# Performance work log

Hardware: AMD Instinct MI355X
Metric: run time of the kernel (lower is better)

## Reference

```python
import jax, jax.numpy as jnp
import numpy as np
import math

B, N, D, H = 4, 2048, 1024, 16
d = D // H
F = 2048                      # field_size
PAD = 8192                    # _next_fast_size(4*F) = 2^13
FB = PAD // 2 + 1             # rfft freq bins
NC = 32                       # spectral-gate control points
EPS = 1e-6                    # feature-map positivity floor


def setup_inputs():
    key = jax.random.key(0)
    ks = jax.random.split(key, 16)
    rn = lambda k, sh, s=0.02: (jax.random.normal(k, sh) * s).astype(jnp.float32)
    eye = jnp.eye(d, dtype=jnp.float32)
    n = jnp.arange(H, dtype=jnp.float32)
    return {
        "x": jax.random.normal(ks[0], (B, N, D), dtype=jnp.float32),
        "w_qkvg": rn(ks[1], (4 * D, D)),
        "b_qkvg": jnp.concatenate([jnp.zeros(3 * D), jnp.full((D,), 2.0)]).astype(jnp.float32),
        "w_out": rn(ks[2], (D, D)),
        "b_out": jnp.zeros((D,), jnp.float32),
        "qfm_w": jnp.stack([eye + rn(ks[3], (d, d)), eye + rn(ks[4], (d, d))]),
        "qfm_b": jnp.zeros((2, d), jnp.float32),
        "kfm_w": jnp.stack([eye + rn(ks[5], (d, d)), eye + rn(ks[6], (d, d))]),
        "kfm_b": jnp.zeros((2, d), jnp.float32),
        "wg_w": rn(ks[7], (1, d)),
        "wg_b": jnp.zeros((1,), jnp.float32),
        "ln_g": jnp.ones((d,), jnp.float32),
        "ln_b": jnp.zeros((d,), jnp.float32),
        "sg_w1": rn(ks[8], (D, D)),
        "sg_b1": jnp.zeros((D,), jnp.float32),
        "sg_w2": rn(ks[9], (H * NC, D), 0.001),
        "sg_b2": jnp.zeros((H * NC,), jnp.float32),
        "wave_freq": (math.pi * (2 * n + 1) / 2).astype(jnp.float32),
        "wave_damp": jnp.full((H,), -0.69, jnp.float32),
        "wave_phase": jnp.linspace(0.0, math.pi, H).astype(jnp.float32),
        "coupling": (jnp.eye(H, dtype=jnp.float32) + rn(ks[10], (H, H), 0.01)),
    }


def _featmap(x, w, b):
    # Hedgehog-style learned positive feature map: depth x (Linear -> ReLU), + eps
    for i in range(w.shape[0]):
        x = jax.nn.relu(x @ w[i].T + b[i])
    return x + EPS


def reference(x, w_qkvg, b_qkvg, w_out, b_out, qfm_w, qfm_b, kfm_w, kfm_b,
              wg_w, wg_b, ln_g, ln_b, sg_w1, sg_b1, sg_w2, sg_b2,
              wave_freq, wave_damp, wave_phase, coupling):
    # fused qkvg projection -> per-head tensors (B,H,N,d)
    qkvg = x @ w_qkvg.T + b_qkvg
    q, k, v, g = [t.reshape(B, N, H, d).transpose(0, 2, 1, 3)
                  for t in jnp.split(qkvg, 4, axis=-1)]
    phi_q = _featmap(q, qfm_w, qfm_b)
    phi_k = _featmap(k, kfm_w, kfm_b)
    wg = jax.nn.sigmoid(k @ wg_w.T + wg_b)  # (B,H,N,1) write gate

    # token -> field position mapping (cached buffers in the original)
    stride = (F - 1) / max(N - 1, 1)
    pos = jnp.clip(jnp.arange(N, dtype=jnp.float32) * stride, 0, F - 2)
    lo = jnp.clip(pos.astype(jnp.int32), 0, F - 2)
    hi = lo + 1
    frac = jnp.clip(pos - lo.astype(jnp.float32), 0.0, 1.0)

    # scatter numerator (gated phi_k*v) + denominator (gated phi_k) streams
    write = jnp.concatenate([wg * phi_k * v, wg * phi_k], axis=-1)  # (B,H,N,2d)
    field = jnp.zeros((B, H, F, 2 * d), jnp.float32)
    field = field.at[:, :, lo, :].add(write * (1.0 - frac)[:, None])
    field = field.at[:, :, hi, :].add(write * frac[:, None])

    # left-aligned causal damped-wave kernel per head
    t = jnp.arange(F, dtype=jnp.float32) / F
    kern = jnp.exp(-jnp.exp(wave_damp)[:, None] * t) * \
           jnp.cos(wave_freq[:, None] * t + wave_phase[:, None])  # (H,F)
    base_fft = jnp.fft.rfft(kern, n=PAD, axis=-1)                 # (H,FB) complex

    # content-adaptive spectral gate from token 0 (causally safe)
    q0 = q[:, :, 0, :]
    mu = q0.mean(-1, keepdims=True)
    var = q0.var(-1, keepdims=True)
    q0 = (q0 - mu) / jnp.sqrt(var + 1e-5) * ln_g + ln_b
    h1 = jax.nn.gelu(q0.reshape(B, H * d) @ sg_w1.T + sg_b1)
    ctrl = (h1 @ sg_w2.T + sg_b2).reshape(B, H, NC)
    ip = jnp.arange(FB, dtype=jnp.float32) * (NC - 1) / (FB - 1)  # align_corners=True
    il = jnp.clip(ip.astype(jnp.int32), 0, NC - 2)
    iw = ip - il.astype(jnp.float32)
    gate = ctrl[:, :, il] * (1.0 - iw) + ctrl[:, :, il + 1] * iw  # (B,H,FB)
    mod = base_fft[None] * (1.0 + gate)                           # (B,H,FB) complex

    # FFT-domain global convolution + head coupling
    conv = jnp.fft.irfft(jnp.fft.rfft(field, n=PAD, axis=2) * mod[..., None],
                         n=PAD, axis=2)[:, :, :F, :]
    conv = jnp.einsum('hg,bgfc->bhfc', coupling, conv)

    # linear-interp read-back at token positions
    y = conv[:, :, lo, :] * (1.0 - frac)[:, None] + conv[:, :, hi, :] * frac[:, None]
    y_num, y_den = y[..., :d], y[..., d:]
    den = jnp.abs(jnp.sum(phi_q * y_den, axis=-1, keepdims=True)) + 1e-4
    out_h = (phi_q * y_num / den) * jax.nn.sigmoid(g)
    return out_h.transpose(0, 2, 1, 3).reshape(B, N, D) @ w_out.T + b_out
```

## Files before the change

### kernel.cpp

```cpp
#include <hip/hip_runtime.h>
#include <math.h>

#define B_   4
#define N_   2048
#define D_   1024
#define H_   16
#define d_   64
#define F_   2048
#define PAD_ 8192
#define FB_  4097
#define NC_  32
#define EPS_ 1e-6f
#define PI_F 3.14159265358979323846f
#define PI_D 3.14159265358979323846

typedef unsigned short ushort_t;
typedef short bf16x8 __attribute__((ext_vector_type(8)));
typedef float f32x4  __attribute__((ext_vector_type(4)));

#define GLD16(gp, lp) __builtin_amdgcn_global_load_lds( \
    (const __attribute__((address_space(1))) unsigned int*)(const void*)(gp), \
    (__attribute__((address_space(3))) unsigned int*)(void*)(lp), 16, 0, 0)

__device__ __forceinline__ ushort_t bf16_rne(float v) {
    unsigned b = __float_as_uint(v);
    unsigned rb = b + 0x7fffu + ((b >> 16) & 1u);
    return (ushort_t)(rb >> 16);
}
__device__ __forceinline__ void split_bf16(float v, ushort_t& h, ushort_t& l) {
    h = bf16_rne(v);
    float fh = __uint_as_float((unsigned)h << 16);
    l = bf16_rne(v - fh);
}

__device__ __forceinline__ float2 cmul(float2 a, float2 w) {
    return make_float2(a.x * w.x - a.y * w.y, a.x * w.y + a.y * w.x);
}
__device__ __forceinline__ float2 cmulc(float2 a, float2 w) {
    return make_float2(a.x * w.x + a.y * w.y, a.y * w.x - a.x * w.y);
}

__global__ __launch_bounds__(256) void kern_twid(float2* __restrict__ twid,
                                                 float2* __restrict__ tw4) {
    int idx = blockIdx.x * 256 + threadIdx.x;
    if (idx < 13 * 4096) {
        const int lh = idx >> 12, t = idx & 4095;
        const int hh = 1 << lh;
        const int j = t & (hh - 1);
        double s, c;
        sincos(-PI_D * (double)j / (double)hh, &s, &c);
        twid[idx] = make_float2((float)c, (float)s);
    } else {
        idx -= 13 * 4096;
        if (idx < 6 * 3072) {
            const int s = idx / 3072;
            const int r = idx - s * 3072;
            const int j = r / 3;
            const int m = r - 3 * j + 1;
            const int q = 1024 >> (2 * s);
            double sn, cs;
            sincos(-2.0 * PI_D * (double)(m * (j & (q - 1))) / (double)(4 * q), &sn, &cs);
            tw4[idx] = make_float2((float)cs, (float)sn);
        }
    }
}

__global__ __launch_bounds__(256) void kern_split3(
        const float* __restrict__ s0, ushort_t* __restrict__ h0, ushort_t* __restrict__ l0, int n0,
        const float* __restrict__ s1, ushort_t* __restrict__ h1, ushort_t* __restrict__ l1, int n1,
        const float* __restrict__ s2, ushort_t* __restrict__ h2, ushort_t* __restrict__ l2, int n2) {
    int i = blockIdx.x * 256 + threadIdx.x;
    const float* s; ushort_t* hh; ushort_t* ll; int k;
    if (i < n0)                { s = s0; hh = h0; ll = l0; k = i; }
    else if (i < n0 + n1)      { s = s1; hh = h1; ll = l1; k = i - n0; }
    else if (i < n0 + n1 + n2) { s = s2; hh = h2; ll = l2; k = i - n0 - n1; }
    else return;
    ushort_t h, l;
    split_bf16(s[k], h, l);
    hh[k] = h; ll[k] = l;
}

__global__ __launch_bounds__(256) void gemm_mfma(
        const ushort_t* __restrict__ Ah, const ushort_t* __restrict__ Al, int lda,
        const ushort_t* __restrict__ Bh, const ushort_t* __restrict__ Bl, int ldb,
        const float* __restrict__ bias, float* __restrict__ C,
        int Nn, int K) {
    __shared__ __align__(16) ushort_t At0[128 * 32];
    __shared__ __align__(16) ushort_t At1[128 * 32];
    __shared__ __align__(16) ushort_t Bt0[128 * 32];
    __shared__ __align__(16) ushort_t Bt1[128 * 32];

    const int tid = threadIdx.x;
    const int wv = tid >> 6, lane = tid & 63;
    const int quad = lane >> 4, lrow = lane & 15;
    const int m0 = blockIdx.y * 128, n0 = blockIdx.x * 128;
    const int mw = (wv >> 1) * 64, nw = (wv & 1) * 64;

    const int srow = lane >> 2;
    const int schunk = (((lane & 3) ^ ((lane >> 3) & 3)) * 8);
    const int qsw = ((quad ^ ((lrow >> 1) & 3)) * 8);

    f32x4 acc[4][4] = {};

    for (int k0 = 0; k0 < K; k0 += 32) {
        {
            const size_t ga = (size_t)(m0 + wv * 32 + srow) * lda + k0 + schunk;
            const size_t gb = (size_t)(n0 + wv * 32 + srow) * ldb + k0 + schunk;
            const size_t ga2 = ga + (size_t)16 * lda;
            const size_t gb2 = gb + (size_t)16 * ldb;
            GLD16(Ah + ga,  &At0[(wv * 32) * 32]);
            GLD16(Ah + ga2, &At0[(wv * 32 + 16) * 32]);
            GLD16(Al + ga,  &At1[(wv * 32) * 32]);
            GLD16(Al + ga2, &At1[(wv * 32 + 16) * 32]);
            GLD16(Bh + gb,  &Bt0[(wv * 32) * 32]);
            GLD16(Bh + gb2, &Bt0[(wv * 32 + 16) * 32]);
            GLD16(Bl + gb,  &Bt1[(wv * 32) * 32]);
            GLD16(Bl + gb2, &Bt1[(wv * 32 + 16) * 32]);
        }
        __syncthreads();

        bf16x8 a0[4], a1[4], b0[4], b1[4];
#pragma unroll
        for (int i = 0; i < 4; ++i) {
            a0[i] = *(const bf16x8*)&At0[(mw + i * 16 + lrow) * 32 + qsw];
            a1[i] = *(const bf16x8*)&At1[(mw + i * 16 + lrow) * 32 + qsw];
            b0[i] = *(const bf16x8*)&Bt0[(nw + i * 16 + lrow) * 32 + qsw];
            b1[i] = *(const bf16x8*)&Bt1[(nw + i * 16 + lrow) * 32 + qsw];
        }
#pragma unroll
        for (int mi = 0; mi < 4; ++mi)
#pragma unroll
            for (int nj = 0; nj < 4; ++nj) {
                acc[mi][nj] = __builtin_amdgcn_mfma_f32_16x16x32_bf16(a0[mi], b0[nj], acc[mi][nj], 0, 0, 0);
                acc[mi][nj] = __builtin_amdgcn_mfma_f32_16x16x32_bf16(a0[mi], b1[nj], acc[mi][nj], 0, 0, 0);
                acc[mi][nj] = __builtin_amdgcn_mfma_f32_16x16x32_bf16(a1[mi], b0[nj], acc[mi][nj], 0, 0, 0);
            }
        __syncthreads();
    }

#pragma unroll
    for (int mi = 0; mi < 4; ++mi) {
        const int row = m0 + mw + mi * 16 + quad * 4;
#pragma unroll
        for (int nj = 0; nj < 4; ++nj) {
            const int col = n0 + nw + nj * 16 + lrow;
            const float bv = bias[col];
#pragma unroll
            for (int r = 0; r < 4; ++r)
                C[(size_t)(row + r) * Nn + col] = acc[mi][nj][r] + bv;
        }
    }
}

__device__ __forceinline__ float gelu_f(float x) {
    return 0.5f * x * (1.f + tanhf(0.7978845608028654f * (x + 0.044715f * x * x * x)));
}

__global__ __launch_bounds__(256) void kern_gemv4(const float* __restrict__ A,
                                                  const float* __restrict__ W,
                                                  const float* __restrict__ bias,
                                                  float* __restrict__ C,
                                                  int Nn, int act) {
    const int tid = threadIdx.x;
    const int wv = tid >> 6, lane = tid & 63;
    const int col = blockIdx.x * 4 + wv;
    const float* wp = W + (size_t)col * D_;
    float a0 = 0.f, a1 = 0.f, a2 = 0.f, a3 = 0.f;
#pragma unroll
    for (int i = 0; i < 16; ++i) {
        int k = lane + i * 64;
        float w = wp[k];
        a0 += A[k] * w;
        a1 += A[D_ + k] * w;
        a2 += A[2 * D_ + k] * w;
        a3 += A[3 * D_ + k] * w;
    }
    for (int m = 1; m < 64; m <<= 1) {
        a0 += __shfl_xor(a0, m);
        a1 += __shfl_xor(a1, m);
        a2 += __shfl_xor(a2, m);
        a3 += __shfl_xor(a3, m);
    }
    if (lane == 0) {
        float bv = bias[col];
        float v0 = a0 + bv, v1 = a1 + bv, v2 = a2 + bv, v3 = a3 + bv;
        if (act) { v0 = gelu_f(v0); v1 = gelu_f(v1); v2 = gelu_f(v2); v3 = gelu_f(v3); }
        C[0 * Nn + col] = v0;
        C[1 * Nn + col] = v1;
        C[2 * Nn + col] = v2;
        C[3 * Nn + col] = v3;
    }
}

__global__ __launch_bounds__(256) void kern_feat(float* __restrict__ qkvg,
                                                 const float* __restrict__ qfm_w,
                                                 const float* __restrict__ qfm_b,
                                                 const float* __restrict__ kfm_w,
                                                 const float* __restrict__ kfm_b,
                                                 const float* __restrict__ wg_w,
                                                 const float* __restrict__ wg_b,
                                                 float* __restrict__ field) {
    __shared__ __align__(16) float in_t[64][68];
    __shared__ __align__(16) float tmp[64][68];
    __shared__ __align__(16) float wbuf[64][68];
    __shared__ __align__(16) float bsm[64];
    __shared__ float wsm[64];
    __shared__ float wgbuf[64];

    const int tid = threadIdx.x;
    const int lane = tid & 63, grp = tid >> 6;
    const int n0 = blockIdx.x * 64;
    const int h = blockIdx.y, b = blockIdx.z;
    const size_t rowbase = (size_t)(b * N_ + n0) * 4096;

    const int lr4 = tid >> 4;
    const int lc4 = (tid & 15) * 4;

    const int rg = lane >> 4;
    const int cg4 = (lane & 15) * 4;
    const int rbase = grp * 16 + rg * 4;

#define LOAD64x64(dst, off) \
    for (int it = 0; it < 4; ++it) { \
        int r = lr4 + it * 16; \
        float4 v = *(const float4*)&qkvg[rowbase + (size_t)r * 4096 + (off) + lc4]; \
        *(float4*)&dst[r][lc4] = v; \
    }

#define MLP2_ACC(srcarr) \
    f32x4 acc[4] = {}; \
    for (int c4 = 0; c4 < 64; c4 += 4) { \
        f32x4 wv0 = *(const f32x4*)&wbuf[c4 + 0][cg4]; \
        f32x4 wv1 = *(const f32x4*)&wbuf[c4 + 1][cg4]; \
        f32x4 wv2 = *(const f32x4*)&wbuf[c4 + 2][cg4]; \
        f32x4 wv3 = *(const f32x4*)&wbuf[c4 + 3][cg4]; \
        _Pragma("unroll") for (int rr = 0; rr < 4; ++rr) { \
            f32x4 iv = *(const f32x4*)&srcarr[rbase + rr][c4]; \
            acc[rr] += wv0 * iv[0]; \
            acc[rr] += wv1 * iv[1]; \
            acc[rr] += wv2 * iv[2]; \
            acc[rr] += wv3 * iv[3]; \
        } \
    }

#define MLP2_STORE_LDS(dstarr, EPSV) { \
    f32x4 b4 = *(const f32x4*)&bsm[cg4]; \
    _Pragma("unroll") for (int rr = 0; rr < 4; ++rr) { \
        f32x4 v = acc[rr] + b4; \
        _Pragma("unroll") for (int k = 0; k < 4; ++k) v[k] = fmaxf(v[k], 0.f) + (EPSV); \
        *(f32x4*)&dstarr[rbase + rr][cg4] = v; } }

    LOAD64x64(in_t, D_ + h * 64)
    for (int it = 0; it < 16; ++it) {
        int r = grp + 4 * it;
        wbuf[lane][r] = kfm_w[(size_t)r * 64 + lane];
    }
    if (tid < 64) { bsm[tid] = kfm_b[tid]; wsm[tid] = wg_w[tid]; }
    __syncthreads();
    if (tid < 64) {
        float s = 0.f;
        for (int c4 = 0; c4 < 64; c4 += 4) {
            float4 iv = *(const float4*)&in_t[tid][c4];
            s += iv.x * wsm[c4] + iv.y * wsm[c4 + 1] + iv.z * wsm[c4 + 2] + iv.w * wsm[c4 + 3];
        }
        s += wg_b[0];
        wgbuf[tid] = 1.f / (1.f + expf(-s));
    }
    {
        MLP2_ACC(in_t)
        MLP2_STORE_LDS(tmp, 0.f)
    }
    __syncthreads();
    for (int it = 0; it < 16; ++it) {
        int r = grp + 4 * it;
        wbuf[lane][r] = kfm_w[(size_t)(64 + r) * 64 + lane];
    }
    if (tid < 64) bsm[tid] = kfm_b[64 + tid];
    __syncthreads();
    {
        MLP2_ACC(tmp)
        MLP2_STORE_LDS(in_t, EPS_)
    }
    __syncthreads();
    LOAD64x64(tmp, 2 * D_ + h * 64)
    __syncthreads();

    {
        float* frow = field + (size_t)(b * H_ + h) * 128 * F_;
        const bool last = (n0 == N_ - 64);
        for (int c = grp; c < 128; c += 4) {
            int i = lane;
            float v = (c < 64) ? wgbuf[i] * in_t[i][c] * tmp[i][c]
                               : wgbuf[i] * in_t[i][c - 64];
            if (last) {
                if (i == 62) {
                    float v2 = (c < 64) ? wgbuf[63] * in_t[63][c] * tmp[63][c]
                                        : wgbuf[63] * in_t[63][c - 64];
                    v += v2;
                } else if (i == 63) v = 0.f;
            }
            frow[(size_t)c * F_ + n0 + i] = v;
        }
    }
    __syncthreads();

    LOAD64x64(in_t, h * 64)
    for (int it = 0; it < 16; ++it) {
        int r = grp + 4 * it;
        wbuf[lane][r] = qfm_w[(size_t)r * 64 + lane];
    }
    if (tid < 64) bsm[tid] = qfm_b[tid];
    __syncthreads();
    {
        MLP2_ACC(in_t)
        MLP2_STORE_LDS(tmp, 0.f)
    }
    __syncthreads();
    for (int it = 0; it < 16; ++it) {
        int r = grp + 4 * it;
        wbuf[lane][r] = qfm_w[(size_t)(64 + r) * 64 + lane];
    }
    if (tid < 64) bsm[tid] = qfm_b[64 + tid];
    __syncthreads();
    {
        MLP2_ACC(tmp)
        f32x4 b4 = *(const f32x4*)&bsm[cg4];
#pragma unroll
        for (int rr = 0; rr < 4; ++rr) {
            f32x4 v = acc[rr] + b4;
#pragma unroll
            for (int k = 0; k < 4; ++k) v[k] = fmaxf(v[k], 0.f) + EPS_;
            *(f32x4*)&qkvg[rowbase + (size_t)(rbase + rr) * 4096 + D_ + h * 64 + cg4] = v;
        }
    }
#undef LOAD64x64
#undef MLP2_ACC
#undef MLP2_STORE_LDS
}

__global__ void kern_ln(const float* __restrict__ qkvg,
                        const float* __restrict__ ln_g,
                        const float* __restrict__ ln_b,
                        float* __restrict__ q0n) {
    const int bh = blockIdx.x, c = threadIdx.x;
    const int b = bh >> 4, h = bh & 15;
    float x = qkvg[(size_t)(b * N_) * 4096 + h * 64 + c];
    float mu = x;
    for (int m = 1; m < 64; m <<= 1) mu += __shfl_xor(mu, m);
    mu *= (1.f / 64.f);
    float dv = (x - mu) * (x - mu);
    for (int m = 1; m < 64; m <<= 1) dv += __shfl_xor(dv, m);
    float var = dv * (1.f / 64.f);
    q0n[b * 1024 + h * 64 + c] = (x - mu) * rsqrtf(var + 1e-5f) * ln_g[c] + ln_b[c];
}

template <int NT>
__device__ __forceinline__ void fft_fwd_dif_t(float* xr, float* xi, int tid, int logn,
                                              const float2* __restrict__ twid) {
    const int nb = 1 << (logn - 1);
    for (int lh = logn - 1; lh >= 0; --lh) {
        const int hh = 1 << lh;
        const float2* tws = twid + lh * 4096;
        for (int t = tid; t < nb; t += NT) {
            int j = t & (hh - 1);
            int i1 = ((t >> lh) << (lh + 1)) | j;
            int i2 = i1 + hh;
            float2 tw = tws[t];
            float ar = xr[i1], ai = xi[i1];
            float br = xr[i2], bi = xi[i2];
            xr[i1] = ar + br; xi[i1] = ai + bi;
            float tr = ar - br, ti = ai - bi;
            xr[i2] = tr * tw.x - ti * tw.y;
            xi[i2] = tr * tw.y + ti * tw.x;
        }
        __syncthreads();
    }
}

template <int NT>
__device__ __forceinline__ void fft_inv_dit_t(float* xr, float* xi, int tid, int logn,
                                              const float2* __restrict__ twid) {
    const int nb = 1 << (logn - 1);
    for (int lh = 0; lh < logn; ++lh) {
        const int hh = 1 << lh;
        const float2* tws = twid + lh * 4096;
        for (int t = tid; t < nb; t += NT) {
            int j = t & (hh - 1);
            int i1 = ((t >> lh) << (lh + 1)) | j;
            int i2 = i1 + hh;
            float2 tw = tws[t];
            float br = xr[i2], bi = xi[i2];
            float tr = br * tw.x + bi * tw.y;
            float ti = bi * tw.x - br * tw.y;
            float ar = xr[i1], ai = xi[i1];
            xr[i1] = ar + tr; xi[i1] = ai + ti;
            xr[i2] = ar - tr; xi[i2] = ai - ti;
        }
        __syncthreads();
    }
}

#define ZIDX(i) ((i) + ((i) >> 4))

template <int NT, int SBEG, int SEND>
__device__ __forceinline__ void fft4_fwd_stages(float2* z, int tid,
                                                const float2* __restrict__ tw4) {
#pragma unroll
    for (int s = SBEG; s < SEND; ++s) {
        const int q = 1024 >> (2 * s);
        const int qq = q + (q >> 4);
        const float2* tws = tw4 + s * 3072;
        for (int t = tid; t < 1024; t += NT) {
            int j = t & (q - 1);
            int base = ((t & ~(q - 1)) << 2) | j;
            int i0, i1, i2, i3;
            if (q >= 16) { i0 = ZIDX(base); i1 = i0 + qq; i2 = i1 + qq; i3 = i2 + qq; }
            else { i0 = ZIDX(base); i1 = ZIDX(base + q); i2 = ZIDX(base + 2 * q); i3 = ZIDX(base + 3 * q); }
            float2 a = z[i0], b = z[i1], c = z[i2], d = z[i3];
            float2 s0 = make_float2(a.x + c.x, a.y + c.y);
            float2 s1 = make_float2(a.x - c.x, a.y - c.y);
            float2 s2 = make_float2(b.x + d.x, b.y + d.y);
            float2 s3 = make_float2(b.x - d.x, b.y - d.y);
            float2 m1 = make_float2(s1.x + s3.y, s1.y - s3.x);
            float2 m2 = make_float2(s0.x - s2.x, s0.y - s2.y);
            float2 m3 = make_float2(s1.x - s3.y, s1.y + s3.x);
            z[i0] = make_float2(s0.x + s2.x, s0.y + s2.y);
            z[i1] = cmul(m1, tws[3 * j + 0]);
            z[i2] = cmul(m2, tws[3 * j + 1]);
            z[i3] = cmul(m3, tws[3 * j + 2]);
        }
        __syncthreads();
    }
}

template <int NT>
__device__ __forceinline__ void fft4_inv(float2* z, int tid,
                                         const float2* __restrict__ tw4) {
#pragma unroll
    for (int s = 5; s >= 0; --s) {
        const int q = 1024 >> (2 * s);
        const int qq = q + (q >> 4);
        const float2* tws = tw4 + s * 3072;
        for (int t = tid; t < 1024; t += NT) {
            int j = t & (q - 1);
            int base = ((t & ~(q - 1)) << 2) | j;
            int i0, i1, i2, i3;
            if (q >= 16) { i0 = ZIDX(base); i1 = i0 + qq; i2 = i1 + qq; i3 = i2 + qq; }
            else { i0 = ZIDX(base); i1 = ZIDX(base + q); i2 = ZIDX(base + 2 * q); i3 = ZIDX(base + 3 * q); }
            float2 a = z[i0];
            float2 b = cmulc(z[i1], tws[3 * j + 0]);
            float2 c = cmulc(z[i2], tws[3 * j + 1]);
            float2 d = cmulc(z[i3], tws[3 * j + 2]);
            float2 p0 = make_float2(a.x + c.x, a.y + c.y);
            float2 p1 = make_float2(a.x - c.x, a.y - c.y);
            float2 p2 = make_float2(b.x + d.x, b.y + d.y);
            float2 p3 = make_float2(b.x - d.x, b.y - d.y);
            z[i0] = make_float2(p0.x + p2.x, p0.y + p2.y);
            z[i1] = make_float2(p1.x - p3.y, p1.y + p3.x);
            z[i2] = make_float2(p0.x - p2.x, p0.y - p2.y);
            z[i3] = make_float2(p1.x + p3.y, p1.y - p3.x);
        }
        __syncthreads();
    }
}

__global__ __launch_bounds__(1024) void kern_prep(const float* __restrict__ freq,
                                                  const float* __restrict__ damp,
                                                  const float* __restrict__ phase,
                                                  const float* __restrict__ ctrl,
                                                  const float2* __restrict__ twid,
                                                  const float2* __restrict__ tw4,
                                                  float* __restrict__ GBR) {
    __shared__ float sm[2 * PAD_];
    float* xr = sm;
    float* xi = sm + PAD_;
    const int bh = blockIdx.x, tid = threadIdx.x;
    const int b = bh >> 4, h = bh & 15;

    const float fr = freq[h], ed = expf(damp[h]), ph = phase[h];
    for (int f = tid; f < PAD_; f += 1024) {
        float v = 0.f;
        if (f < F_) {
            float t = (float)f / (float)F_;
            v = expf(-ed * t) * cosf(fr * t + ph);
        }
        xr[f] = v; xi[f] = 0.f;
    }
    __syncthreads();
    fft_fwd_dif_t<1024>(xr, xi, tid, 13, twid);

    const float* cp = ctrl + b * (H_ * NC_) + h * NC_;
    for (int j = tid; j < PAD_; j += 1024) {
        int k = (int)(__brev((unsigned)j) >> 19);
        int kk = min(k, PAD_ - k);
        float ip = (float)kk * ((float)(NC_ - 1) / (float)(FB_ - 1));
        int il = min((int)ip, NC_ - 2);
        float iw = ip - (float)il;
        float m = 1.f + cp[il] * (1.f - iw) + cp[il + 1] * iw;
        xr[j] *= m;
        xi[j] *= m;
    }
    __syncthreads();
    fft_inv_dit_t<1024>(xr, xi, tid, 13, twid);

    float g[4];
    const float sc = 1.f / (float)PAD_;
#pragma unroll
    for (int u = 0; u < 4; ++u) {
        int j = tid + u * 1024;
        g[u] = ((j < 2048) ? xr[j] : xr[j + 4096]) * sc;
    }
    __syncthreads();
    float2* z = (float2*)sm;
#pragma unroll
    for (int u = 0; u < 4; ++u) {
        int j = tid + u * 1024;
        z[ZIDX(j)] = make_float2(g[u], 0.f);
    }
    __syncthreads();
    fft4_fwd_stages<1024, 0, 5>(z, tid, tw4);
    {
        const float sc2 = 1.f / 4096.f;
        const int t = tid;
        const int base = t << 2;
        float2 a = z[ZIDX(base)], bq = z[ZIDX(base + 1)];
        float2 c = z[ZIDX(base + 2)], dq = z[ZIDX(base + 3)];
        float2 s0 = make_float2(a.x + c.x, a.y + c.y);
        float2 s1 = make_float2(a.x - c.x, a.y - c.y);
        float2 s2 = make_float2(bq.x + dq.x, bq.y + dq.y);
        float2 s3 = make_float2(bq.x - dq.x, bq.y - dq.y);
        float2 o0 = make_float2(s0.x + s2.x, s0.y + s2.y);
        float2 o1 = make_float2(s1.x + s3.y, s1.y - s3.x);
        float2 o2 = make_float2(s0.x - s2.x, s0.y - s2.y);
        float2 o3 = make_float2(s1.x - s3.y, s1.y + s3.x);
        float2* Gp = (float2*)GBR + (size_t)bh * 4096 + base;
        Gp[0] = make_float2(o0.x * sc2, o0.y * sc2);
        Gp[1] = make_float2(o1.x * sc2, o1.y * sc2);
        Gp[2] = make_float2(o2.x * sc2, o2.y * sc2);
        Gp[3] = make_float2(o3.x * sc2, o3.y * sc2);
    }
}

__global__ __launch_bounds__(512) void kern_conv4(float* __restrict__ field,
                                                  const float* __restrict__ GBR,
                                                  const float2* __restrict__ tw4) {
    __shared__ float2 z[4351];
    const int tid = threadIdx.x;
    const int bh = blockIdx.x >> 6, cp = blockIdx.x & 63;
    float* rowx = field + ((size_t)bh * 128 + 2 * cp) * F_;
    float* rowy = rowx + F_;

    for (int f = tid; f < 2048; f += 512)
        z[ZIDX(f)] = make_float2(rowx[f], rowy[f]);
    __syncthreads();

    {
        const float2* tws = tw4;
        for (int t = tid; t < 1024; t += 512) {
            int i0 = ZIDX(t), i1 = i0 + 1088, i2 = i1 + 1088, i3 = i2 + 1088;
            float2 a = z[i0], b = z[i1];
            float2 m1 = make_float2(a.x + b.y, a.y - b.x);
            float2 m2 = make_float2(a.x - b.x, a.y - b.y);
            float2 m3 = make_float2(a.x - b.y, a.y + b.x);
            z[i0] = make_float2(a.x + b.x, a.y + b.y);
            z[i1] = cmul(m1, tws[3 * t + 0]);
            z[i2] = cmul(m2, tws[3 * t + 1]);
            z[i3] = cmul(m3, tws[3 * t + 2]);
        }
        __syncthreads();
    }

    fft4_fwd_stages<512, 1, 5>(z, tid, tw4);

    {
        const float2* G = (const float2*)(GBR) + (size_t)bh * 4096;
        for (int t = tid; t < 1024; t += 512) {
            int base = t << 2;
            int i0 = ZIDX(base), i1 = ZIDX(base + 1), i2 = ZIDX(base + 2), i3 = ZIDX(base + 3);
            float2 a = z[i0], b = z[i1], c = z[i2], d = z[i3];
            float2 s0 = make_float2(a.x + c.x, a.y + c.y);
            float2 s1 = make_float2(a.x - c.x, a.y - c.y);
            float2 s2 = make_float2(b.x + d.x, b.y + d.y);
            float2 s3 = make_float2(b.x - d.x, b.y - d.y);
            float2 o0 = make_float2(s0.x + s2.x, s0.y + s2.y);
            float2 o1 = make_float2(s1.x + s3.y, s1.y - s3.x);
            float2 o2 = make_float2(s0.x - s2.x, s0.y - s2.y);
            float2 o3 = make_float2(s1.x - s3.y, s1.y + s3.x);
            z[i0] = cmul(o0, G[base + 0]);
            z[i1] = cmul(o1, G[base + 1]);
            z[i2] = cmul(o2, G[base + 2]);
            z[i3] = cmul(o3, G[base + 3]);
        }
        __syncthreads();
    }

    fft4_inv<512>(z, tid, tw4);

    for (int f = tid; f < 2048; f += 512) {
        float2 v = z[ZIDX(f)];
        rowx[f] = v.x;
        rowy[f] = v.y;
    }
}

__global__ __launch_bounds__(1024) void kern_combine(float* __restrict__ qkvg,
                                                     const float* __restrict__ field,
                                                     const float* __restrict__ coupling) {
    __shared__ float cpl[16][16];
    __shared__ float sbuf[2][128][17];
    const int tid = threadIdx.x;
    if (tid < 256) cpl[tid >> 4][tid & 15] = coupling[tid];
    const int lane = tid & 63, wv = tid >> 6;
    const int n = blockIdx.x * 16 + wv;
    const int b = blockIdx.y;
    const int f0 = blockIdx.x * 16;
    const int fi = min(n, F_ - 2) - f0;
    const size_t row = (size_t)(b * N_ + n) * 4096;

    const int lc = tid >> 3, lk = (tid & 7) * 2;
    const float* fb = field + (size_t)b * 16 * 128 * F_;

    float2 rv = *(const float2*)&fb[(size_t)lc * F_ + f0 + lk];
    __syncthreads();
    sbuf[0][lc][lk] = rv.x; sbuf[0][lc][lk + 1] = rv.y;

    float ynum[16], yden[16];
#pragma unroll
    for (int hh = 0; hh < 16; ++hh) { ynum[hh] = 0.f; yden[hh] = 0.f; }

    for (int g = 0; g < 16; ++g) {
        if (g < 15)
            rv = *(const float2*)&fb[((size_t)(g + 1) * 128 + lc) * F_ + f0 + lk];
        __syncthreads();
        const float nv = sbuf[g & 1][lane][fi];
        const float dv = sbuf[g & 1][64 + lane][fi];
#pragma unroll
        for (int hh = 0; hh < 16; ++hh) {
            const float cg = cpl[hh][g];
            ynum[hh] += cg * nv;
            yden[hh] += cg * dv;
        }
        if (g < 15) { sbuf[(g + 1) & 1][lc][lk] = rv.x; sbuf[(g + 1) & 1][lc][lk + 1] = rv.y; }
    }

    ushort_t* rp = (ushort_t*)(qkvg + row);
#pragma unroll
    for (int hh = 0; hh < 16; ++hh) {
        float pq = qkvg[row + D_ + hh * 64 + lane];
        float gv = qkvg[row + 3 * D_ + hh * 64 + lane];
        float s = pq * yden[hh];
        for (int m = 1; m < 64; m <<= 1) s += __shfl_xor(s, m);
        float den = fabsf(s) + 1e-4f;
        float o = pq * ynum[hh] / den * (1.f / (1.f + expf(-gv)));
        ushort_t oh, ol;
        split_bf16(o, oh, ol);
        rp[hh * 64 + lane] = oh;
        rp[1024 + hh * 64 + lane] = ol;
    }
}

extern "C" void kernel_launch(void* const* d_in, const int* in_sizes, int n_in,
                              void* d_out, int out_size, void* d_ws, size_t ws_size,
                              hipStream_t stream) {
    const float* x      = (const float*)d_in[0];
    const float* w_qkvg = (const float*)d_in[1];
    const float* b_qkvg = (const float*)d_in[2];
    const float* w_out  = (const float*)d_in[3];
    const float* b_out  = (const float*)d_in[4];
    const float* qfm_w  = (const float*)d_in[5];
    const float* qfm_b  = (const float*)d_in[6];
    const float* kfm_w  = (const float*)d_in[7];
    const float* kfm_b  = (const float*)d_in[8];
    const float* wg_w   = (const float*)d_in[9];
    const float* wg_b   = (const float*)d_in[10];
    const float* ln_g   = (const float*)d_in[11];
    const float* ln_b   = (const float*)d_in[12];
    const float* sg_w1  = (const float*)d_in[13];
    const float* sg_b1  = (const float*)d_in[14];
    const float* sg_w2  = (const float*)d_in[15];
    const float* sg_b2  = (const float*)d_in[16];
    const float* wfreq  = (const float*)d_in[17];
    const float* wdamp  = (const float*)d_in[18];
    const float* wphase = (const float*)d_in[19];
    const float* coup   = (const float*)d_in[20];

    float* ws = (float*)d_ws;
    float*  qkvg   = ws;
    float*  field  = ws + 33554432;
    float*  GBR    = ws + 50593792;
    float2* twid   = (float2*)(ws + 51118080);
    float*  q0n    = ws + 51224576;
    float*  h1     = ws + 51228672;
    float*  ctrl   = ws + 51232768;
    ushort_t* wouth = (ushort_t*)(ws + 51234816);
    ushort_t* woutl = (ushort_t*)(ws + 51759104);
    float2* tw4    = (float2*)(ws + 52283392);

    ushort_t* xh  = (ushort_t*)(field);
    ushort_t* xl  = (ushort_t*)(field + 4194304);
    ushort_t* wqh = (ushort_t*)(field + 8388608);
    ushort_t* wql = (ushort_t*)(field + 10485760);

    kern_twid<<<(13 * 4096 + 6 * 3072) / 256, 256, 0, stream>>>(twid, tw4);
    kern_split3<<<(B_ * N_ * D_ + 4 * D_ * D_ + D_ * D_) / 256, 256, 0, stream>>>(
        x, xh, xl, B_ * N_ * D_,
        w_qkvg, wqh, wql, 4 * D_ * D_,
        w_out, wouth, woutl, D_ * D_);

    for (int l = 0; l < 4; ++l) {
        const size_t aoff = (size_t)l * 2048 * D_;
        gemm_mfma<<<dim3(4096 / 128, 2048 / 128), 256, 0, stream>>>(
            xh + aoff, xl + aoff, D_, wqh, wql, D_, b_qkvg,
            qkvg + (size_t)l * 2048 * 4096, 4 * D_, D_);
    }

    kern_ln<<<B_ * H_, 64, 0, stream>>>(qkvg, ln_g, ln_b, q0n);
    kern_gemv4<<<D_ / 4, 256, 0, stream>>>(q0n, sg_w1, sg_b1, h1, D_, 1);
    kern_gemv4<<<(H_ * NC_) / 4, 256, 0, stream>>>(h1, sg_w2, sg_b2, ctrl, H_ * NC_, 0);

    kern_prep<<<B_ * H_, 1024, 0, stream>>>(wfreq, wdamp, wphase, ctrl, twid, tw4, GBR);

    kern_feat<<<dim3(N_ / 64, H_, B_), 256, 0, stream>>>(
        qkvg, qfm_w, qfm_b, kfm_w, kfm_b, wg_w, wg_b, field);

    kern_conv4<<<B_ * H_ * 64, 512, 0, stream>>>(field, GBR, tw4);

    kern_combine<<<dim3(N_ / 16, B_), 1024, 0, stream>>>(qkvg, field, coup);

    gemm_mfma<<<dim3(1024 / 128, 8192 / 128), 256, 0, stream>>>(
        (ushort_t*)qkvg, (ushort_t*)qkvg + 1024, 8192,
        wouth, woutl, D_, b_out, (float*)d_out, D_, D_);
}
```

Baseline: 705.9 us.

## Restructure FFT convolution as register-resident radix-16 passes with fewer LDS syncs

The 4096-point FFT convolution kernel now keeps 16 complex values per thread in registers and fuses pairs of radix-4 stages into radix-16 passes. This cuts the number of shared-memory round trips and barriers from about 14 to 5, and the spectral multiply is folded into the middle pass. LDS padding is replaced with an XOR swizzle, and the block size drops from 512 to 256 threads. In exchange, register pressure per thread is higher, which could lower occupancy.

```diff
diff --git a/kernel.cpp b/kernel.cpp
--- a/kernel.cpp
+++ b/kernel.cpp
@@ -433,35 +433,57 @@
     }
 }
 
-template <int NT>
-__device__ __forceinline__ void fft4_inv(float2* z, int tid,
-                                         const float2* __restrict__ tw4) {
-#pragma unroll
-    for (int s = 5; s >= 0; --s) {
-        const int q = 1024 >> (2 * s);
-        const int qq = q + (q >> 4);
-        const float2* tws = tw4 + s * 3072;
-        for (int t = tid; t < 1024; t += NT) {
-            int j = t & (q - 1);
-            int base = ((t & ~(q - 1)) << 2) | j;
-            int i0, i1, i2, i3;
-            if (q >= 16) { i0 = ZIDX(base); i1 = i0 + qq; i2 = i1 + qq; i3 = i2 + qq; }
-            else { i0 = ZIDX(base); i1 = ZIDX(base + q); i2 = ZIDX(base + 2 * q); i3 = ZIDX(base + 3 * q); }
-            float2 a = z[i0];
-            float2 b = cmulc(z[i1], tws[3 * j + 0]);
-            float2 c = cmulc(z[i2], tws[3 * j + 1]);
-            float2 d = cmulc(z[i3], tws[3 * j + 2]);
-            float2 p0 = make_float2(a.x + c.x, a.y + c.y);
-            float2 p1 = make_float2(a.x - c.x, a.y - c.y);
-            float2 p2 = make_float2(b.x + d.x, b.y + d.y);
-            float2 p3 = make_float2(b.x - d.x, b.y - d.y);
-            z[i0] = make_float2(p0.x + p2.x, p0.y + p2.y);
-            z[i1] = make_float2(p1.x - p3.y, p1.y + p3.x);
-            z[i2] = make_float2(p0.x - p2.x, p0.y - p2.y);
-            z[i3] = make_float2(p1.x + p3.y, p1.y - p3.x);
-        }
-        __syncthreads();
-    }
+__device__ __forceinline__ void bf4_fwd(float2& e0, float2& e1, float2& e2, float2& e3,
+                                        const float2* __restrict__ tws, int j) {
+    float2 a = e0, b = e1, c = e2, d = e3;
+    float2 s0 = make_float2(a.x + c.x, a.y + c.y);
+    float2 s1 = make_float2(a.x - c.x, a.y - c.y);
+    float2 s2 = make_float2(b.x + d.x, b.y + d.y);
+    float2 s3 = make_float2(b.x - d.x, b.y - d.y);
+    float2 m1 = make_float2(s1.x + s3.y, s1.y - s3.x);
+    float2 m2 = make_float2(s0.x - s2.x, s0.y - s2.y);
+    float2 m3 = make_float2(s1.x - s3.y, s1.y + s3.x);
+    e0 = make_float2(s0.x + s2.x, s0.y + s2.y);
+    e1 = cmul(m1, tws[3 * j + 0]);
+    e2 = cmul(m2, tws[3 * j + 1]);
+    e3 = cmul(m3, tws[3 * j + 2]);
+}
+__device__ __forceinline__ void bf4_fwd_id(float2& e0, float2& e1, float2& e2, float2& e3) {
+    float2 a = e0, b = e1, c = e2, d = e3;
+    float2 s0 = make_float2(a.x + c.x, a.y + c.y);
+    float2 s1 = make_float2(a.x - c.x, a.y - c.y);
+    float2 s2 = make_float2(b.x + d.x, b.y + d.y);
+    float2 s3 = make_float2(b.x - d.x, b.y - d.y);
+    e0 = make_float2(s0.x + s2.x, s0.y + s2.y);
+    e1 = make_float2(s1.x + s3.y, s1.y - s3.x);
+    e2 = make_float2(s0.x - s2.x, s0.y - s2.y);
+    e3 = make_float2(s1.x - s3.y, s1.y + s3.x);
+}
+__device__ __forceinline__ void bf4_inv(float2& e0, float2& e1, float2& e2, float2& e3,
+                                        const float2* __restrict__ tws, int j) {
+    float2 a = e0;
+    float2 b = cmulc(e1, tws[3 * j + 0]);
+    float2 c = cmulc(e2, tws[3 * j + 1]);
+    float2 d = cmulc(e3, tws[3 * j + 2]);
+    float2 p0 = make_float2(a.x + c.x, a.y + c.y);
+    float2 p1 = make_float2(a.x - c.x, a.y - c.y);
+    float2 p2 = make_float2(b.x + d.x, b.y + d.y);
+    float2 p3 = make_float2(b.x - d.x, b.y - d.y);
+    e0 = make_float2(p0.x + p2.x, p0.y + p2.y);
+    e1 = make_float2(p1.x - p3.y, p1.y + p3.x);
+    e2 = make_float2(p0.x - p2.x, p0.y - p2.y);
+    e3 = make_float2(p1.x + p3.y, p1.y - p3.x);
+}
+__device__ __forceinline__ void bf4_inv_id(float2& e0, float2& e1, float2& e2, float2& e3) {
+    float2 a = e0, b = e1, c = e2, d = e3;
+    float2 p0 = make_float2(a.x + c.x, a.y + c.y);
+    float2 p1 = make_float2(a.x - c.x, a.y - c.y);
+    float2 p2 = make_float2(b.x + d.x, b.y + d.y);
+    float2 p3 = make_float2(b.x - d.x, b.y - d.y);
+    e0 = make_float2(p0.x + p2.x, p0.y + p2.y);
+    e1 = make_float2(p1.x - p3.y, p1.y + p3.x);
+    e2 = make_float2(p0.x - p2.x, p0.y - p2.y);
+    e3 = make_float2(p1.x + p3.y, p1.y - p3.x);
 }
 
 __global__ __launch_bounds__(1024) void kern_prep(const float* __restrict__ freq,
@@ -541,65 +563,113 @@
     }
 }
 
-__global__ __launch_bounds__(512) void kern_conv4(float* __restrict__ field,
+#define LIDX(i) ((i) ^ (((i) >> 4) & 15))
+
+__global__ __launch_bounds__(256) void kern_conv4(float* __restrict__ field,
                                                   const float* __restrict__ GBR,
                                                   const float2* __restrict__ tw4) {
-    __shared__ float2 z[4351];
+    __shared__ float2 z[4096];
     const int tid = threadIdx.x;
     const int bh = blockIdx.x >> 6, cp = blockIdx.x & 63;
     float* rowx = field + ((size_t)bh * 128 + 2 * cp) * F_;
     float* rowy = rowx + F_;
-
-    for (int f = tid; f < 2048; f += 512)
-        z[ZIDX(f)] = make_float2(rowx[f], rowy[f]);
-    __syncthreads();
-
-    {
-        const float2* tws = tw4;
-        for (int t = tid; t < 1024; t += 512) {
-            int i0 = ZIDX(t), i1 = i0 + 1088, i2 = i1 + 1088, i3 = i2 + 1088;
-            float2 a = z[i0], b = z[i1];
-            float2 m1 = make_float2(a.x + b.y, a.y - b.x);
-            float2 m2 = make_float2(a.x - b.x, a.y - b.y);
-            float2 m3 = make_float2(a.x - b.y, a.y + b.x);
-            z[i0] = make_float2(a.x + b.x, a.y + b.y);
-            z[i1] = cmul(m1, tws[3 * t + 0]);
-            z[i2] = cmul(m2, tws[3 * t + 1]);
-            z[i3] = cmul(m3, tws[3 * t + 2]);
-        }
-        __syncthreads();
-    }
-
-    fft4_fwd_stages<512, 1, 5>(z, tid, tw4);
-
-    {
-        const float2* G = (const float2*)(GBR) + (size_t)bh * 4096;
-        for (int t = tid; t < 1024; t += 512) {
-            int base = t << 2;
-            int i0 = ZIDX(base), i1 = ZIDX(base + 1), i2 = ZIDX(base + 2), i3 = ZIDX(base + 3);
-            float2 a = z[i0], b = z[i1], c = z[i2], d = z[i3];
-            float2 s0 = make_float2(a.x + c.x, a.y + c.y);
-            float2 s1 = make_float2(a.x - c.x, a.y - c.y);
-            float2 s2 = make_float2(b.x + d.x, b.y + d.y);
-            float2 s3 = make_float2(b.x - d.x, b.y - d.y);
-            float2 o0 = make_float2(s0.x + s2.x, s0.y + s2.y);
-            float2 o1 = make_float2(s1.x + s3.y, s1.y - s3.x);
-            float2 o2 = make_float2(s0.x - s2.x, s0.y - s2.y);
-            float2 o3 = make_float2(s1.x - s3.y, s1.y + s3.x);
-            z[i0] = cmul(o0, G[base + 0]);
-            z[i1] = cmul(o1, G[base + 1]);
-            z[i2] = cmul(o2, G[base + 2]);
-            z[i3] = cmul(o3, G[base + 3]);
-        }
-        __syncthreads();
-    }
-
-    fft4_inv<512>(z, tid, tw4);
-
-    for (int f = tid; f < 2048; f += 512) {
-        float2 v = z[ZIDX(f)];
-        rowx[f] = v.x;
-        rowy[f] = v.y;
+    const float2* tws0 = tw4;
+    const float2* tws1 = tw4 + 3072;
+    const float2* tws2 = tw4 + 2 * 3072;
+    const float2* tws3 = tw4 + 3 * 3072;
+    const float2* tws4s = tw4 + 4 * 3072;
+
+    float2 x[16];
+
+    {
+        const int j16 = tid;
+#pragma unroll
+        for (int m = 0; m < 8; ++m)
+            x[m] = make_float2(rowx[j16 + 256 * m], rowy[j16 + 256 * m]);
+#pragma unroll
+        for (int m = 8; m < 16; ++m) x[m] = make_float2(0.f, 0.f);
+#pragma unroll
+        for (int r = 0; r < 4; ++r)
+            bf4_fwd(x[r], x[r + 4], x[r + 8], x[r + 12], tws0, j16 + 256 * r);
+#pragma unroll
+        for (int c = 0; c < 4; ++c)
+            bf4_fwd(x[4 * c], x[4 * c + 1], x[4 * c + 2], x[4 * c + 3], tws1, j16);
+#pragma unroll
+        for (int m = 0; m < 16; ++m) z[LIDX(j16 + 256 * m)] = x[m];
+    }
+    __syncthreads();
+
+    {
+        const int j16 = tid & 15;
+        const int pb = (tid >> 4) * 256 + j16;
+#pragma unroll
+        for (int m = 0; m < 16; ++m) x[m] = z[LIDX(pb + 16 * m)];
+#pragma unroll
+        for (int r = 0; r < 4; ++r)
+            bf4_fwd(x[r], x[r + 4], x[r + 8], x[r + 12], tws2, j16 + 16 * r);
+#pragma unroll
+        for (int c = 0; c < 4; ++c)
+            bf4_fwd(x[4 * c], x[4 * c + 1], x[4 * c + 2], x[4 * c + 3], tws3, j16);
+#pragma unroll
+        for (int m = 0; m < 16; ++m) z[LIDX(pb + 16 * m)] = x[m];
+    }
+    __syncthreads();
+
+    {
+        const int pb = tid * 16;
+#pragma unroll
+        for (int m = 0; m < 16; ++m) x[m] = z[LIDX(pb + m)];
+#pragma unroll
+        for (int r = 0; r < 4; ++r)
+            bf4_fwd(x[r], x[r + 4], x[r + 8], x[r + 12], tws4s, r);
+#pragma unroll
+        for (int c = 0; c < 4; ++c)
+            bf4_fwd_id(x[4 * c], x[4 * c + 1], x[4 * c + 2], x[4 * c + 3]);
+        const float2* G = (const float2*)GBR + (size_t)bh * 4096 + pb;
+#pragma unroll
+        for (int m = 0; m < 16; ++m) x[m] = cmul(x[m], G[m]);
+#pragma unroll
+        for (int c = 0; c < 4; ++c)
+            bf4_inv_id(x[4 * c], x[4 * c + 1], x[4 * c + 2], x[4 * c + 3]);
+#pragma unroll
+        for (int r = 0; r < 4; ++r)
+            bf4_inv(x[r], x[r + 4], x[r + 8], x[r + 12], tws4s, r);
+#pragma unroll
+        for (int m = 0; m < 16; ++m) z[LIDX(pb + m)] = x[m];
+    }
+    __syncthreads();
+
+    {
+        const int j16 = tid & 15;
+        const int pb = (tid >> 4) * 256 + j16;
+#pragma unroll
+        for (int m = 0; m < 16; ++m) x[m] = z[LIDX(pb + 16 * m)];
+#pragma unroll
+        for (int c = 0; c < 4; ++c)
+            bf4_inv(x[4 * c], x[4 * c + 1], x[4 * c + 2], x[4 * c + 3], tws3, j16);
+#pragma unroll
+        for (int r = 0; r < 4; ++r)
+            bf4_inv(x[r], x[r + 4], x[r + 8], x[r + 12], tws2, j16 + 16 * r);
+#pragma unroll
+        for (int m = 0; m < 16; ++m) z[LIDX(pb + 16 * m)] = x[m];
+    }
+    __syncthreads();
+
+    {
+        const int j16 = tid;
+#pragma unroll
+        for (int m = 0; m < 16; ++m) x[m] = z[LIDX(j16 + 256 * m)];
+#pragma unroll
+        for (int c = 0; c < 4; ++c)
+            bf4_inv(x[4 * c], x[4 * c + 1], x[4 * c + 2], x[4 * c + 3], tws1, j16);
+#pragma unroll
+        for (int r = 0; r < 4; ++r)
+            bf4_inv(x[r], x[r + 4], x[r + 8], x[r + 12], tws0, j16 + 256 * r);
+#pragma unroll
+        for (int m = 0; m < 8; ++m) {
+            rowx[j16 + 256 * m] = x[m].x;
+            rowy[j16 + 256 * m] = x[m].y;
+        }
     }
 }
 
@@ -723,7 +793,7 @@
     kern_feat<<<dim3(N_ / 64, H_, B_), 256, 0, stream>>>(
         qkvg, qfm_w, qfm_b, kfm_w, kfm_b, wg_w, wg_b, field);
 
-    kern_conv4<<<B_ * H_ * 64, 512, 0, stream>>>(field, GBR, tw4);
+    kern_conv4<<<B_ * H_ * 64, 256, 0, stream>>>(field, GBR, tw4);
 
     kern_combine<<<dim3(N_ / 16, B_), 1024, 0, stream>>>(qkvg, field, coup);
 
```

Measured after the change: 684.4 us. -3.1%, faster.
